# Kernel optimization log

Hardware: AMD Instinct MI355X
Metric: run time of the kernel (lower is better)

## Reference

```python
import jax, jax.numpy as jnp
import numpy as np

ALPHA = 0.2  # LeakyReLU slope
NEG = -1e9


def setup_inputs() -> dict:
    key = jax.random.key(0)
    k1, k2, k3, k4, k5 = jax.random.split(key, 5)
    B, N, F_IN, F_OUT, H = 8, 1024, 512, 256, 8
    x = jax.random.normal(k1, (B, N, F_IN), dtype=jnp.float32)
    adj = jax.random.randint(k2, (B, N, N), 0, 2, dtype=jnp.int32)
    W = jax.random.normal(k3, (H, F_OUT, F_IN), dtype=jnp.float32) * 0.05
    a1 = jax.random.normal(k4, (H, F_OUT), dtype=jnp.float32) * 0.05
    a2 = jax.random.normal(k5, (H, F_OUT), dtype=jnp.float32) * 0.05
    return {"x": x, "adj": adj, "W": W, "a1": a1, "a2": a2}


def _head(x, adj_zero, W, a1, a2):
    # x: (B,N,F_in), W: (F_out,F_in), a1/a2: (F_out,)
    h = jnp.einsum('bnf,of->bno', x, W)              # (B,N,F_out)
    f1 = jnp.einsum('bno,o->bn', h, a1)              # (B,N)
    f2 = jnp.einsum('bno,o->bn', h, a2)              # (B,N)
    e = f1[:, :, None] + f2[:, None, :]              # (B,N,N) broadcast add
    e = jax.nn.leaky_relu(e, negative_slope=ALPHA)
    e = jnp.where(adj_zero, NEG, e)                  # adjacency mask
    att = jax.nn.softmax(e, axis=2)
    return jnp.einsum('bnm,bmo->bno', att, h)        # (B,N,F_out)


def reference(x, adj, W, a1, a2):
    adj_zero = (adj == 0)
    # vmap over heads; sum of elu(head outputs)
    heads = jax.vmap(lambda w, u, v: _head(x, adj_zero, w, u, v))(W, a1, a2)  # (H,B,N,F_out)
    out = jnp.sum(jax.nn.elu(heads), axis=0)         # (B,N,F_out)
    return jax.nn.log_softmax(out, axis=2)
```

## Files before the change

kernel.cpp:

```cpp
#include <hip/hip_runtime.h>
#include <math.h>

#define B_    8
#define N_    1024
#define FIN   512
#define FOUT  256
#define H_    8
#define ALPHA 0.2f

#define XT (B_ * N_ * FIN)
#define WT (H_ * FOUT * FIN)

typedef short s16x8 __attribute__((ext_vector_type(8)));
typedef float f32x4 __attribute__((ext_vector_type(4)));

__device__ __forceinline__ unsigned short f2bf(float f) {
  unsigned int u = __float_as_uint(f);
  u = (u + 0x7FFFu + ((u >> 16) & 1u)) >> 16;
  return (unsigned short)u;
}

__device__ __forceinline__ unsigned int pk4_fp8(float a, float b, float c,
                                                float d) {
  int u = __builtin_amdgcn_cvt_pk_fp8_f32(a, b, 0, false);
  u = __builtin_amdgcn_cvt_pk_fp8_f32(c, d, u, true);
  return (unsigned int)u;
}


#define CVB  ((XT + WT) / 1024)
#define ZRB  128
#define PKB  ((B_ * N_ * 32) / 256)

__global__ __launch_bounds__(256) void prep(
    const float* __restrict__ x, const float* __restrict__ W,
    const int* __restrict__ adj, unsigned short* __restrict__ xb,
    unsigned short* __restrict__ Wb, float* __restrict__ f12,
    unsigned int* __restrict__ adjP) {
  const int blk = blockIdx.x;
  if (blk >= CVB + ZRB) {
    const int dw = (blk - CVB - ZRB) * 256 + threadIdx.x;
    const int r = dw >> 5, pd = dw & 31;
    const int q = pd >> 3, c8 = pd & 7;
    const int* ap = adj + (size_t)r * N_;
    unsigned int out = 0;
#pragma unroll
    for (int i = 0; i < 4; ++i) {
      const int jb = (c8 * 4 + i) * 32 + q * 8;
      int4 v0 = *(const int4*)(ap + jb);
      int4 v1 = *(const int4*)(ap + jb + 4);
      unsigned int byte = 0;
      byte |= (v0.x ? 1u : 0u) << 0; byte |= (v0.y ? 1u : 0u) << 1;
      byte |= (v0.z ? 1u : 0u) << 2; byte |= (v0.w ? 1u : 0u) << 3;
      byte |= (v1.x ? 1u : 0u) << 4; byte |= (v1.y ? 1u : 0u) << 5;
      byte |= (v1.z ? 1u : 0u) << 6; byte |= (v1.w ? 1u : 0u) << 7;
      out |= byte << (i * 8);
    }
    adjP[dw] = out;
    return;
  }
  if (blk >= CVB) {
    const int i = (blk - CVB) * 256 + threadIdx.x;
    ((float4*)f12)[i] = make_float4(0.f, 0.f, 0.f, 0.f);
    return;
  }
  const int i = (blk * 256 + threadIdx.x) * 4;
  const float* src;
  unsigned short* dst;
  int off;
  if (i < XT) { src = x; dst = xb; off = i; }
  else        { src = W; dst = Wb; off = i - XT; }
  float4 v = *(const float4*)(src + off);
  ushort4 s;
  s.x = f2bf(v.x); s.y = f2bf(v.y); s.z = f2bf(v.z); s.w = f2bf(v.w);
  *(ushort4*)(dst + off) = s;
}

__global__ __launch_bounds__(256) void proj_mfma(
    const unsigned short* __restrict__ xb, const unsigned short* __restrict__ Wb,
    const float* __restrict__ a1, const float* __restrict__ a2,
    unsigned char* __restrict__ htq, float* __restrict__ f1,
    float* __restrict__ f2) {
  __shared__ __align__(16) unsigned short As[128 * 64];
  __shared__ __align__(16) unsigned short Bs[64 * 64];
  const int gid = blockIdx.x;
  const int b = gid & 7;
  const int mt_ = (gid >> 3) & 7;
  const int ot_ = (gid >> 6) & 3;
  const int h = gid >> 8;
  const int hb = h * B_ + b;
  const int m0 = mt_ * 128, o0 = ot_ * 64;
  const int t = threadIdx.x, w = t >> 6, lane = t & 63;
  const int col = lane & 15, quad = lane >> 4;

  const int srow = t >> 3;
  const int sslot = t & 7;
  const int sseg = sslot ^ (srow & 7);
  const unsigned short* agp = xb + (size_t)(b * N_ + m0 + srow) * FIN + sseg * 8;
  const unsigned short* bgp = Wb + (size_t)(h * FOUT + o0 + srow) * FIN + sseg * 8;

  f32x4 acc[2][4];
  const f32x4 z4 = {0.f, 0.f, 0.f, 0.f};
#pragma unroll
  for (int mt = 0; mt < 2; ++mt)
#pragma unroll
    for (int ot = 0; ot < 4; ++ot) acc[mt][ot] = z4;

  s16x8 pa[4], pb[2];
#pragma unroll
  for (int i2 = 0; i2 < 4; ++i2) pa[i2] = *(const s16x8*)(agp + (size_t)i2 * 32 * FIN);
#pragma unroll
  for (int i2 = 0; i2 < 2; ++i2) pb[i2] = *(const s16x8*)(bgp + (size_t)i2 * 32 * FIN);

  for (int it = 0; it < FIN / 64; ++it) {
    __syncthreads();
#pragma unroll
    for (int i2 = 0; i2 < 4; ++i2)
      *(s16x8*)&As[(i2 * 32 + srow) * 64 + sslot * 8] = pa[i2];
#pragma unroll
    for (int i2 = 0; i2 < 2; ++i2)
      *(s16x8*)&Bs[(i2 * 32 + srow) * 64 + sslot * 8] = pb[i2];
    __syncthreads();
    if (it < FIN / 64 - 1) {
      const int k0 = (it + 1) * 64;
#pragma unroll
      for (int i2 = 0; i2 < 4; ++i2)
        pa[i2] = *(const s16x8*)(agp + (size_t)i2 * 32 * FIN + k0);
#pragma unroll
      for (int i2 = 0; i2 < 2; ++i2)
        pb[i2] = *(const s16x8*)(bgp + (size_t)i2 * 32 * FIN + k0);
    }
#pragma unroll
    for (int kb = 0; kb < 2; ++kb) {
      s16x8 af[2], bf[4];
#pragma unroll
      for (int mt = 0; mt < 2; ++mt) {
        const int row = w * 32 + mt * 16 + col;
        af[mt] = *(const s16x8*)&As[row * 64 + ((kb * 4 + quad) ^ (row & 7)) * 8];
      }
#pragma unroll
      for (int ot = 0; ot < 4; ++ot) {
        const int row = ot * 16 + col;
        bf[ot] = *(const s16x8*)&Bs[row * 64 + ((kb * 4 + quad) ^ (row & 7)) * 8];
      }
#pragma unroll
      for (int mt = 0; mt < 2; ++mt)
#pragma unroll
        for (int ot = 0; ot < 4; ++ot)
          acc[mt][ot] = __builtin_amdgcn_mfma_f32_16x16x32_bf16(af[mt], bf[ot],
                                                                acc[mt][ot], 0, 0, 0);
    }
  }

  const int kkw = (m0 >> 5) + w;
  float pf1[2][4] = {{0.f}}, pf2[2][4] = {{0.f}};
#pragma unroll
  for (int mt = 0; mt < 2; ++mt) {
#pragma unroll
    for (int ot = 0; ot < 4; ++ot) {
      const int o = o0 + ot * 16 + col;
      const float va1 = a1[h * FOUT + o], va2 = a2[h * FOUT + o];
      const int otg = (o0 >> 4) + ot;
      unsigned char* fb =
          htq + (((size_t)(hb * 16 + otg) * 32 + kkw) << 9);
      const unsigned int q =
          pk4_fp8(acc[mt][ot][0], acc[mt][ot][1], acc[mt][ot][2], acc[mt][ot][3]);
      *(unsigned int*)(fb + (2 * mt + (quad >> 1)) * 128 + col * 8 +
                       (quad & 1) * 4) = q;
#pragma unroll
      for (int r = 0; r < 4; ++r) {
        pf1[mt][r] += acc[mt][ot][r] * va1;
        pf2[mt][r] += acc[mt][ot][r] * va2;
      }
    }
  }
#pragma unroll
  for (int off = 1; off <= 8; off <<= 1)
#pragma unroll
    for (int mt = 0; mt < 2; ++mt)
#pragma unroll
      for (int r = 0; r < 4; ++r) {
        pf1[mt][r] += __shfl_xor(pf1[mt][r], off);
        pf2[mt][r] += __shfl_xor(pf2[mt][r], off);
      }
  if (col == 0) {
#pragma unroll
    for (int mt = 0; mt < 2; ++mt)
#pragma unroll
      for (int r = 0; r < 4; ++r) {
        const int n = m0 + w * 32 + mt * 16 + quad * 4 + r;
        atomicAdd(&f1[hb * N_ + n], pf1[mt][r]);
        atomicAdd(&f2[hb * N_ + n], pf2[mt][r]);
      }
  }
}

__global__ __launch_bounds__(256) void wgen(
    const float* __restrict__ f1, const float* __restrict__ f2,
    const unsigned int* __restrict__ adjP, unsigned char* __restrict__ wq) {
  const int id = blockIdx.x;
  const int b = id & 7, h = (id >> 3) & 7;
  const int rbg = (id >> 6) & 15;
  const int kkh = id >> 10;
  const int w = threadIdx.x >> 6, lane = threadIdx.x & 63;
  const int col = lane & 15, quad = lane >> 4;
  const int hb = h * B_ + b;
  const int rb = rbg * 4 + w;
  const int row = rb * 16 + col;

  const float* f2r = f2 + (size_t)hb * N_;
  float m2 = -3.0e38f;
#pragma unroll
  for (int c = 0; c < 16; ++c) m2 = fmaxf(m2, f2r[lane + c * 64]);
#pragma unroll
  for (int off = 32; off; off >>= 1) m2 = fmaxf(m2, __shfl_xor(m2, off));

  const float f1i = f1[(size_t)hb * N_ + row];
  const float tb = f1i + m2;
  const float mhat = fmaxf(tb, ALPHA * tb);

  const unsigned int* adp = adjP + ((size_t)(b * N_ + row) << 5) + quad * 8;
  const float* f2p = f2r + quad * 8;
  unsigned char* wp = wq + (((size_t)(hb * 64 + rb) * 32) << 9) + lane * 8;

#pragma unroll
  for (int k4i = 0; k4i < 4; ++k4i) {
    const int k4 = kkh * 4 + k4i;
    const unsigned int ad = adp[k4];
#pragma unroll
    for (int k2 = 0; k2 < 4; ++k2) {
      const int kk = k4 * 4 + k2;
      const unsigned int ab = (ad >> (k2 * 8)) & 0xFFu;
      const float4 fA = *(const float4*)(f2p + kk * 32);
      const float4 fB = *(const float4*)(f2p + kk * 32 + 4);
      float ex[8];
#pragma unroll
      for (int j = 0; j < 8; ++j) {
        const float fv = j < 4 ? ((const float*)&fA)[j]
                               : ((const float*)&fB)[j - 4];
        const float tt = f1i + fv;
        const float l = fmaxf(tt, ALPHA * tt);
        const float p = __expf(l - mhat);
        ex[j] = ((ab >> j) & 1u) ? p : 0.f;
      }
      const unsigned int lo = pk4_fp8(ex[0], ex[1], ex[2], ex[3]);
      const unsigned int hi = pk4_fp8(ex[4], ex[5], ex[6], ex[7]);
      *(uint2*)(wp + kk * 512) = make_uint2(lo, hi);
    }
  }
}

__global__ __launch_bounds__(256, 4) void pv(
    const unsigned char* __restrict__ htq, const unsigned char* __restrict__ wq,
    float* __restrict__ p0, float* __restrict__ p1, float* __restrict__ p2,
    float* __restrict__ p3) {
  const int id = blockIdx.x;
  const int b = id & 7;
  const int g0 = (id >> 3) & 3;
  const int oq = (id >> 5) & 3;
  const int it = id >> 7;
  const int w = threadIdx.x >> 6, lane = threadIdx.x & 63;
  const int col = lane & 15, quad = lane >> 4;
  const int rb = it * 8 + w * 2;

  float hsum[2][4][4];
#pragma unroll
  for (int g = 0; g < 2; ++g)
#pragma unroll
    for (int t = 0; t < 4; ++t)
#pragma unroll
      for (int r = 0; r < 4; ++r) hsum[g][t][r] = 0.f;

  const long ones = 0x3838383838383838L;

  for (int hh = 0; hh < 2; ++hh) {
    const int hb = (g0 * 2 + hh) * B_ + b;
    const unsigned char* ap =
        wq + (((size_t)(hb * 64 + rb) * 32) << 9) + lane * 8;
    const unsigned char* bp =
        htq + (((size_t)(hb * 16 + oq * 4) * 32) << 9) + lane * 8;

    f32x4 acc[2][4], accs[2];
    const f32x4 z4 = {0.f, 0.f, 0.f, 0.f};
#pragma unroll
    for (int g = 0; g < 2; ++g) {
      accs[g] = z4;
#pragma unroll
      for (int t = 0; t < 4; ++t) acc[g][t] = z4;
    }

#pragma unroll 2
    for (int kk = 0; kk < 32; ++kk) {
      const long af0 = *(const long*)(ap + kk * 512);
      const long af1 = *(const long*)(ap + 16384 + kk * 512);
      accs[0] = __builtin_amdgcn_mfma_f32_16x16x32_fp8_fp8(af0, ones, accs[0], 0, 0, 0);
      accs[1] = __builtin_amdgcn_mfma_f32_16x16x32_fp8_fp8(af1, ones, accs[1], 0, 0, 0);
#pragma unroll
      for (int t = 0; t < 4; ++t) {
        const long bf = *(const long*)(bp + ((t * 32 + kk) << 9));
        acc[0][t] = __builtin_amdgcn_mfma_f32_16x16x32_fp8_fp8(af0, bf,
                                                               acc[0][t], 0, 0, 0);
        acc[1][t] = __builtin_amdgcn_mfma_f32_16x16x32_fp8_fp8(af1, bf,
                                                               acc[1][t], 0, 0, 0);
      }
    }

#pragma unroll
    for (int g = 0; g < 2; ++g)
#pragma unroll
      for (int r = 0; r < 4; ++r) {
        const float inv = 1.0f / accs[g][r];
#pragma unroll
        for (int t = 0; t < 4; ++t) {
          const float oh = acc[g][t][r] * inv;
          hsum[g][t][r] += oh > 0.f ? oh : __expf(oh) - 1.f;
        }
      }
  }

  float* pdst = (g0 == 0) ? p0 : (g0 == 1) ? p1 : (g0 == 2) ? p2 : p3;
#pragma unroll
  for (int g = 0; g < 2; ++g)
#pragma unroll
    for (int t = 0; t < 4; ++t)
#pragma unroll
      for (int r = 0; r < 4; ++r) {
        const int orow = (rb + g) * 16 + quad * 4 + r;
        pdst[(size_t)(b * N_ + orow) * FOUT + oq * 64 + t * 16 + col] =
            hsum[g][t][r];
      }
}

__global__ __launch_bounds__(256) void logsm(
    const float* __restrict__ p0, const float* __restrict__ p1,
    const float* __restrict__ p2, const float* __restrict__ p3,
    float* __restrict__ out) {
  const int row = blockIdx.x * 4 + (threadIdx.x >> 6);
  const int lane = threadIdx.x & 63;
  const size_t base = (size_t)row * FOUT;
  float v[4];
  float m = -3.0e38f;
#pragma unroll
  for (int c = 0; c < 4; ++c) {
    const size_t idx = base + c * 64 + lane;
    v[c] = p0[idx] + p1[idx] + p2[idx] + p3[idx];
    m = fmaxf(m, v[c]);
  }
#pragma unroll
  for (int off = 32; off; off >>= 1) m = fmaxf(m, __shfl_xor(m, off));
  float s = 0.f;
#pragma unroll
  for (int c = 0; c < 4; ++c) s += __expf(v[c] - m);
#pragma unroll
  for (int off = 32; off; off >>= 1) s += __shfl_xor(s, off);
  const float lg = m + logf(s);
#pragma unroll
  for (int c = 0; c < 4; ++c)
    out[base + c * 64 + lane] = v[c] - lg;
}

extern "C" void kernel_launch(void* const* d_in, const int* in_sizes, int n_in,
                              void* d_out, int out_size, void* d_ws,
                              size_t ws_size, hipStream_t stream) {
  const float* x   = (const float*)d_in[0];
  const int*   adj = (const int*)d_in[1];
  const float* W   = (const float*)d_in[2];
  const float* a1  = (const float*)d_in[3];
  const float* a2  = (const float*)d_in[4];
  float* out = (float*)d_out;

  unsigned char* htq = (unsigned char*)d_ws;
  unsigned short* xb = (unsigned short*)(htq + (size_t)H_ * B_ * FOUT * N_);
  unsigned short* Wb = xb + (size_t)XT;
  float* f1 = (float*)(Wb + (size_t)WT);
  float* f2 = f1 + (size_t)H_ * B_ * N_;
  float* part2 = f2 + (size_t)H_ * B_ * N_;
  float* part3 = part2 + (size_t)B_ * N_ * FOUT;
  unsigned int* adjP = (unsigned int*)(part3 + (size_t)B_ * N_ * FOUT);
  unsigned char* wq = (unsigned char*)(adjP + (size_t)B_ * N_ * 32);
  float* part1 = (float*)xb;

  prep<<<CVB + ZRB + PKB, 256, 0, stream>>>(x, W, adj, xb, Wb, f1, adjP);

  proj_mfma<<<2048, 256, 0, stream>>>(xb, Wb, a1, a2, htq, f1, f2);

  wgen<<<2048, 256, 0, stream>>>(f1, f2, adjP, wq);

  pv<<<1024, 256, 0, stream>>>(htq, wq, out, part1, part2, part3);

  logsm<<<(B_ * N_) / 4, 256, 0, stream>>>(out, part1, part2, part3, out);
}
```

Before: 210.8 us.

## Compute softmax denominators in wgen and software-pipeline fp8 MFMA loads in pv

The softmax row sums are now computed in wgen by dequantizing the packed fp8 weights and are atomically added into a new dnm buffer. This removes the extra ones-vector MFMA per k-step in pv. The pv inner loop is restructured with double-buffered register loads (two prefetch groups) and s_setprio around the MFMA bursts, so global loads overlap the matrix ops. The costs are extra dequantize work and atomics in wgen, and ZRB grows to zero the larger workspace.

Result: no change. 210.5 us (-0.1%).

```diff
diff --git a/kernel.cpp b/kernel.cpp
--- a/kernel.cpp
+++ b/kernel.cpp
@@ -27,9 +27,28 @@
   return (unsigned int)u;
 }
 
+#if __has_builtin(__builtin_amdgcn_cvt_pk_f32_fp8)
+#define HAVE_DEQ4 1
+__device__ __forceinline__ float deq4(unsigned int u) {
+  const auto a = __builtin_amdgcn_cvt_pk_f32_fp8((int)u, false);
+  const auto b = __builtin_amdgcn_cvt_pk_f32_fp8((int)u, true);
+  return (a[0] + a[1]) + (b[0] + b[1]);
+}
+#else
+#define HAVE_DEQ4 0
+__device__ __forceinline__ float q8e4m3(float p) {
+  if (p >= 0.015625f) {
+    unsigned int u = __float_as_uint(p);
+    u = (u + 0x7FFFFu + ((u >> 20) & 1u)) & 0xFFF00000u;
+    return __uint_as_float(u);
+  }
+  return (p + 16384.f) - 16384.f;
+}
+#endif
+
 
 #define CVB  ((XT + WT) / 1024)
-#define ZRB  128
+#define ZRB  192
 #define PKB  ((B_ * N_ * 32) / 256)
 
 __global__ __launch_bounds__(256) void prep(
@@ -197,7 +216,8 @@
 
 __global__ __launch_bounds__(256) void wgen(
     const float* __restrict__ f1, const float* __restrict__ f2,
-    const unsigned int* __restrict__ adjP, unsigned char* __restrict__ wq) {
+    const unsigned int* __restrict__ adjP, unsigned char* __restrict__ wq,
+    float* __restrict__ dnm) {
   const int id = blockIdx.x;
   const int b = id & 7, h = (id >> 3) & 7;
   const int rbg = (id >> 6) & 15;
@@ -223,6 +243,7 @@
   const float* f2p = f2r + quad * 8;
   unsigned char* wp = wq + (((size_t)(hb * 64 + rb) * 32) << 9) + lane * 8;
 
+  float dsum = 0.f;
 #pragma unroll
   for (int k4i = 0; k4i < 4; ++k4i) {
     const int k4 = kkh * 4 + k4i;
@@ -245,15 +266,24 @@
       }
       const unsigned int lo = pk4_fp8(ex[0], ex[1], ex[2], ex[3]);
       const unsigned int hi = pk4_fp8(ex[4], ex[5], ex[6], ex[7]);
+#if HAVE_DEQ4
+      dsum += deq4(lo) + deq4(hi);
+#else
+#pragma unroll
+      for (int j = 0; j < 8; ++j) dsum += q8e4m3(ex[j]);
+#endif
       *(uint2*)(wp + kk * 512) = make_uint2(lo, hi);
     }
   }
+  dsum += __shfl_xor(dsum, 16);
+  dsum += __shfl_xor(dsum, 32);
+  if (quad == 0) atomicAdd(&dnm[(size_t)hb * N_ + row], dsum);
 }
 
 __global__ __launch_bounds__(256, 4) void pv(
     const unsigned char* __restrict__ htq, const unsigned char* __restrict__ wq,
-    float* __restrict__ p0, float* __restrict__ p1, float* __restrict__ p2,
-    float* __restrict__ p3) {
+    const float* __restrict__ dnm, float* __restrict__ p0,
+    float* __restrict__ p1, float* __restrict__ p2, float* __restrict__ p3) {
   const int id = blockIdx.x;
   const int b = id & 7;
   const int g0 = (id >> 3) & 3;
@@ -271,45 +301,70 @@
 #pragma unroll
       for (int r = 0; r < 4; ++r) hsum[g][t][r] = 0.f;
 
-  const long ones = 0x3838383838383838L;
-
   for (int hh = 0; hh < 2; ++hh) {
     const int hb = (g0 * 2 + hh) * B_ + b;
     const unsigned char* ap =
         wq + (((size_t)(hb * 64 + rb) * 32) << 9) + lane * 8;
     const unsigned char* bp =
         htq + (((size_t)(hb * 16 + oq * 4) * 32) << 9) + lane * 8;
-
-    f32x4 acc[2][4], accs[2];
+    const float* dr = dnm + (size_t)hb * N_ + quad * 4;
+    const float4 den0 = *(const float4*)(dr + (rb + 0) * 16);
+    const float4 den1 = *(const float4*)(dr + (rb + 1) * 16);
+
+    f32x4 acc[2][4];
     const f32x4 z4 = {0.f, 0.f, 0.f, 0.f};
 #pragma unroll
-    for (int g = 0; g < 2; ++g) {
-      accs[g] = z4;
+    for (int g = 0; g < 2; ++g)
 #pragma unroll
       for (int t = 0; t < 4; ++t) acc[g][t] = z4;
-    }
-
+
+    long xa0, xa1, xb0, xb1, xb2, xb3;
+    long ya0, ya1, yb0, yb1, yb2, yb3;
+
+#define LOADG(P, k)                                                         \
+    do {                                                                    \
+      P##a0 = *(const long*)(ap + (k) * 512);                               \
+      P##a1 = *(const long*)(ap + 16384 + (k) * 512);                       \
+      P##b0 = *(const long*)(bp + ((k) << 9));                              \
+      P##b1 = *(const long*)(bp + ((32 + (k)) << 9));                       \
+      P##b2 = *(const long*)(bp + ((64 + (k)) << 9));                       \
+      P##b3 = *(const long*)(bp + ((96 + (k)) << 9));                       \
+    } while (0)
+
+#define MFMAG(P)                                                            \
+    do {                                                                    \
+      __builtin_amdgcn_s_setprio(1);                                        \
+      acc[0][0] = __builtin_amdgcn_mfma_f32_16x16x32_fp8_fp8(P##a0, P##b0, acc[0][0], 0, 0, 0); \
+      acc[1][0] = __builtin_amdgcn_mfma_f32_16x16x32_fp8_fp8(P##a1, P##b0, acc[1][0], 0, 0, 0); \
+      acc[0][1] = __builtin_amdgcn_mfma_f32_16x16x32_fp8_fp8(P##a0, P##b1, acc[0][1], 0, 0, 0); \
+      acc[1][1] = __builtin_amdgcn_mfma_f32_16x16x32_fp8_fp8(P##a1, P##b1, acc[1][1], 0, 0, 0); \
+      acc[0][2] = __builtin_amdgcn_mfma_f32_16x16x32_fp8_fp8(P##a0, P##b2, acc[0][2], 0, 0, 0); \
+      acc[1][2] = __builtin_amdgcn_mfma_f32_16x16x32_fp8_fp8(P##a1, P##b2, acc[1][2], 0, 0, 0); \
+      acc[0][3] = __builtin_amdgcn_mfma_f32_16x16x32_fp8_fp8(P##a0, P##b3, acc[0][3], 0, 0, 0); \
+      acc[1][3] = __builtin_amdgcn_mfma_f32_16x16x32_fp8_fp8(P##a1, P##b3, acc[1][3], 0, 0, 0); \
+      __builtin_amdgcn_s_setprio(0);                                        \
+    } while (0)
+
+    LOADG(x, 0);
+    LOADG(y, 1);
 #pragma unroll 2
-    for (int kk = 0; kk < 32; ++kk) {
-      const long af0 = *(const long*)(ap + kk * 512);
-      const long af1 = *(const long*)(ap + 16384 + kk * 512);
-      accs[0] = __builtin_amdgcn_mfma_f32_16x16x32_fp8_fp8(af0, ones, accs[0], 0, 0, 0);
-      accs[1] = __builtin_amdgcn_mfma_f32_16x16x32_fp8_fp8(af1, ones, accs[1], 0, 0, 0);
-#pragma unroll
-      for (int t = 0; t < 4; ++t) {
-        const long bf = *(const long*)(bp + ((t * 32 + kk) << 9));
-        acc[0][t] = __builtin_amdgcn_mfma_f32_16x16x32_fp8_fp8(af0, bf,
-                                                               acc[0][t], 0, 0, 0);
-        acc[1][t] = __builtin_amdgcn_mfma_f32_16x16x32_fp8_fp8(af1, bf,
-                                                               acc[1][t], 0, 0, 0);
-      }
-    }
+    for (int kk = 0; kk < 30; kk += 2) {
+      MFMAG(x);
+      LOADG(x, kk + 2);
+      MFMAG(y);
+      LOADG(y, kk + 3);
+    }
+    MFMAG(x);
+    MFMAG(y);
+#undef LOADG
+#undef MFMAG
 
 #pragma unroll
     for (int g = 0; g < 2; ++g)
 #pragma unroll
       for (int r = 0; r < 4; ++r) {
-        const float inv = 1.0f / accs[g][r];
+        const float dv = (g == 0) ? (&den0.x)[r] : (&den1.x)[r];
+        const float inv = 1.0f / dv;
 #pragma unroll
         for (int t = 0; t < 4; ++t) {
           const float oh = acc[g][t][r] * inv;
@@ -374,7 +429,8 @@
   unsigned short* Wb = xb + (size_t)XT;
   float* f1 = (float*)(Wb + (size_t)WT);
   float* f2 = f1 + (size_t)H_ * B_ * N_;
-  float* part2 = f2 + (size_t)H_ * B_ * N_;
+  float* dnm = f2 + (size_t)H_ * B_ * N_;
+  float* part2 = dnm + (size_t)H_ * B_ * N_;
   float* part3 = part2 + (size_t)B_ * N_ * FOUT;
   unsigned int* adjP = (unsigned int*)(part3 + (size_t)B_ * N_ * FOUT);
   unsigned char* wq = (unsigned char*)(adjP + (size_t)B_ * N_ * 32);
@@ -384,9 +440,9 @@
 
   proj_mfma<<<2048, 256, 0, stream>>>(xb, Wb, a1, a2, htq, f1, f2);
 
-  wgen<<<2048, 256, 0, stream>>>(f1, f2, adjP, wq);
-
-  pv<<<1024, 256, 0, stream>>>(htq, wq, out, part1, part2, part3);
+  wgen<<<2048, 256, 0, stream>>>(f1, f2, adjP, wq, dnm);
+
+  pv<<<1024, 256, 0, stream>>>(htq, wq, dnm, out, part1, part2, part3);
 
   logsm<<<(B_ * N_) / 4, 256, 0, stream>>>(out, part1, part2, part3, out);
 }
```
